# Kernel optimization log

Hardware: AMD Instinct MI355X
Metric: run time of the kernel (lower is better)

Reference implementation:

```python
import jax, jax.numpy as jnp
import numpy as np

B, C = 2048, 512          # batch, channels
CHG = 16                  # coarse grid side (16x16 -> N=256)
FHG = 16                  # fine grid side (16x16 -> F=256)
N = CHG * CHG             # coarse_span.total
F = FHG * FHG             # fine_total
K = 4                     # top4 sample mode
LOG_F = float(np.log(F))


def _ln(x, g, b, eps=1e-5):
    m = jnp.mean(x, axis=-1, keepdims=True)
    v = jnp.var(x, axis=-1, keepdims=True)
    return (x - m) * jax.lax.rsqrt(v + eps) * g + b


def _mlp3(x, w1, b1, w2, b2, w3, b3):
    # linear_stack: Linear+gelu, Linear+gelu, Linear (dropout=0 / eval)
    h = jax.nn.gelu(x @ w1 + b1)
    h = jax.nn.gelu(h @ w2 + b2)
    return h @ w3 + b3


def setup_inputs() -> dict:
    key = jax.random.key(0)
    ks = jax.random.split(key, 10)
    s = 0.02
    return {
        'x': jax.random.normal(ks[0], (B, C), jnp.float32),
        'in_g': jnp.ones((C,), jnp.float32), 'in_b': jnp.zeros((C,), jnp.float32),
        'nop_w': jax.random.normal(ks[1], (C, 1), jnp.float32) * s,
        'nop_b': jnp.zeros((1,), jnp.float32),
        'c_w1': jax.random.normal(ks[2], (C, C), jnp.float32) * s,
        'c_b1': jnp.zeros((C,), jnp.float32),
        'c_w2': jax.random.normal(ks[3], (C, C), jnp.float32) * s,
        'c_b2': jnp.zeros((C,), jnp.float32),
        'c_w3': jax.random.normal(ks[4], (C, N), jnp.float32) * s,
        'c_b3': jnp.zeros((N,), jnp.float32),
        'emb': jax.random.normal(ks[5], (N, C), jnp.float32),
        'emb_g': jnp.ones((C,), jnp.float32), 'emb_b': jnp.zeros((C,), jnp.float32),
        'f_w1': jax.random.normal(ks[6], (2 * C, C), jnp.float32) * s,
        'f_b1': jnp.zeros((C,), jnp.float32),
        'f_w2': jax.random.normal(ks[7], (C, C), jnp.float32) * s,
        'f_b2': jnp.zeros((C,), jnp.float32),
        'f_w3': jax.random.normal(ks[8], (C, F), jnp.float32) * s,
        'f_b3': jnp.zeros((F,), jnp.float32),
    }


def reference(x, in_g, in_b, nop_w, nop_b, c_w1, c_b1, c_w2, c_b2, c_w3, c_b3,
              emb, emb_g, emb_b, f_w1, f_b1, f_w2, f_b2, f_w3, f_b3):
    xn = _ln(x, in_g, in_b)                                  # (B,C)
    no_op = xn @ nop_w + nop_b                               # (B,1)
    coarse = _mlp3(xn, c_w1, c_b1, c_w2, c_b2, c_w3, c_b3)   # (B,N)
    _, idx = jax.lax.top_k(coarse, K)                        # (B,K) int32
    e = _ln(emb[idx], emb_g, emb_b)                          # (B,K,C)
    fin = jnp.concatenate([jnp.broadcast_to(xn[:, None, :], (B, K, C)), e], axis=-1)
    fine = _mlp3(fin, f_w1, f_b1, f_w2, f_b2, f_w3, f_b3)    # (B,K,F)
    # scatter value: coarse[b,i] - log F + fine + log F - lse(fine) = coarse[b,i] + log_softmax(fine)
    vals = jnp.take_along_axis(coarse, idx, axis=1)[:, :, None] + jax.nn.log_softmax(fine, axis=-1)
    dense = jnp.broadcast_to((coarse - LOG_F)[:, :, None], (B, N, F))
    dense = dense.at[jnp.arange(B)[:, None], idx].set(vals)  # top-k indices are distinct
    # view (B, ch0, ch1, fh0, fh1) -> permute (0,1,3,2,4) -> flatten
    xname = dense.reshape(B, CHG, CHG, FHG, FHG).transpose(0, 1, 3, 2, 4).reshape(B, -1)
    return jnp.concatenate([no_op, xname], axis=-1)          # (B, 1 + N*F)
```

## Files before the change

### kernel.cpp

```cpp
#include <hip/hip_runtime.h>
#include <math.h>

#define BATCH 2048
#define CH 512
#define N_COARSE 256
#define F_FINE 256
#define K_TOP 4
#define OUT_STRIDE 65537

typedef unsigned short ushort_t;
typedef __bf16 bf16x8 __attribute__((ext_vector_type(8)));
typedef float f32x4 __attribute__((ext_vector_type(4)));

__device__ __forceinline__ float gelu_tanh(float x) {
    float x3 = x * x * x;
    float t = tanhf(0.7978845608028654f * (x + 0.044715f * x3));
    return 0.5f * x * (1.0f + t);
}

__device__ __forceinline__ ushort_t f2bf(float f) {
    unsigned u = __float_as_uint(f);
    unsigned r = (u + 0x7FFF + ((u >> 16) & 1)) >> 16;
    return (ushort_t)r;
}

__global__ __launch_bounds__(256) void ln_noop_kernel(
    const float* __restrict__ x, const float* __restrict__ g, const float* __restrict__ b,
    const float* __restrict__ nop_w, const float* __restrict__ nop_b,
    float* __restrict__ xn, ushort_t* __restrict__ xn_bf, float* __restrict__ out)
{
    int row = blockIdx.x;
    int t = threadIdx.x;
    int lane = t & 63, wave = t >> 6;
    const float* xr = x + (size_t)row * CH;
    float v0 = xr[t], v1 = xr[t + 256];
    float s = v0 + v1, ss = v0 * v0 + v1 * v1;
    #pragma unroll
    for (int off = 32; off; off >>= 1) { s += __shfl_xor(s, off); ss += __shfl_xor(ss, off); }
    __shared__ float red[8];
    if (lane == 0) { red[wave] = s; red[4 + wave] = ss; }
    __syncthreads();
    s = red[0] + red[1] + red[2] + red[3];
    ss = red[4] + red[5] + red[6] + red[7];
    float mean = s * (1.0f / CH);
    float var = ss * (1.0f / CH) - mean * mean;
    float rsq = rsqrtf(var + 1e-5f);
    float xn0 = (v0 - mean) * rsq * g[t] + b[t];
    float xn1 = (v1 - mean) * rsq * g[t + 256] + b[t + 256];
    float* xnr = xn + (size_t)row * CH;
    xnr[t] = xn0; xnr[t + 256] = xn1;
    ushort_t* xbr = xn_bf + (size_t)row * CH;
    xbr[t] = f2bf(xn0); xbr[t + 256] = f2bf(xn1);
    float d = xn0 * nop_w[t] + xn1 * nop_w[t + 256];
    #pragma unroll
    for (int off = 32; off; off >>= 1) d += __shfl_xor(d, off);
    __syncthreads();
    if (lane == 0) red[wave] = d;
    __syncthreads();
    if (t == 0) out[(size_t)row * OUT_STRIDE] = red[0] + red[1] + red[2] + red[3] + nop_b[0];
}

__global__ __launch_bounds__(256) void emb_ln_kernel(
    const float* __restrict__ emb, const float* __restrict__ g, const float* __restrict__ b,
    const int* __restrict__ idx, ushort_t* __restrict__ e_bf)
{
    int blk = blockIdx.x;
    int t = threadIdx.x;
    int lane = t & 63, wave = t >> 6;
    int n = idx[blk];
    const float* er = emb + (size_t)n * CH;
    float v0 = er[t], v1 = er[t + 256];
    float s = v0 + v1, ss = v0 * v0 + v1 * v1;
    #pragma unroll
    for (int off = 32; off; off >>= 1) { s += __shfl_xor(s, off); ss += __shfl_xor(ss, off); }
    __shared__ float red[8];
    if (lane == 0) { red[wave] = s; red[4 + wave] = ss; }
    __syncthreads();
    s = red[0] + red[1] + red[2] + red[3];
    ss = red[4] + red[5] + red[6] + red[7];
    float mean = s * (1.0f / CH);
    float var = ss * (1.0f / CH) - mean * mean;
    float rsq = rsqrtf(var + 1e-5f);
    ushort_t* orow = e_bf + (size_t)blk * CH;
    orow[t] = f2bf((v0 - mean) * rsq * g[t] + b[t]);
    orow[t + 256] = f2bf((v1 - mean) * rsq * g[t + 256] + b[t + 256]);
}

__global__ __launch_bounds__(256) void convT_kernel(
    const float* __restrict__ W, ushort_t* __restrict__ Wt, int Kd, int Nd)
{
    __shared__ float s[32][33];
    int tx = threadIdx.x & 31, ty = threadIdx.x >> 5;
    int n0 = blockIdx.x * 32, k0 = blockIdx.y * 32;
    #pragma unroll
    for (int i = 0; i < 4; ++i) {
        int r = ty + i * 8;
        s[r][tx] = W[(size_t)(k0 + r) * Nd + n0 + tx];
    }
    __syncthreads();
    #pragma unroll
    for (int i = 0; i < 4; ++i) {
        int r = ty + i * 8;
        Wt[(size_t)(n0 + r) * Kd + k0 + tx] = f2bf(s[tx][r]);
    }
}

template<bool GELU>
__global__ __launch_bounds__(256) void gemm_kernel(
    const float* __restrict__ A, const float* __restrict__ W,
    const float* __restrict__ bias, float* __restrict__ Cmat, int M, int Nd, int Kd)
{
    __shared__ float As[16][68];
    __shared__ float Ws[16][68];
    int tid = threadIdx.x;
    int tx = tid & 15, ty = tid >> 4;
    int n0 = blockIdx.x * 64, m0 = blockIdx.y * 64;

    int lm = tid >> 2;
    int lk = (tid & 3) * 4;
    int wn = (tid & 15) * 4;
    int wk = tid >> 4;

    const float* Aptr = A + (size_t)(m0 + lm) * Kd + lk;
    const float* Wptr = W + (size_t)wk * Nd + n0 + wn;

    float acc[4][4] = {};

    for (int k0 = 0; k0 < Kd; k0 += 16) {
        float4 av = *(const float4*)(Aptr + k0);
        float4 wv = *(const float4*)(Wptr + (size_t)k0 * Nd);
        As[lk + 0][lm] = av.x; As[lk + 1][lm] = av.y;
        As[lk + 2][lm] = av.z; As[lk + 3][lm] = av.w;
        *(float4*)&Ws[wk][wn] = wv;
        __syncthreads();
        #pragma unroll
        for (int kk = 0; kk < 16; ++kk) {
            float4 a = *(const float4*)&As[kk][ty * 4];
            float4 w = *(const float4*)&Ws[kk][tx * 4];
            acc[0][0] += a.x * w.x; acc[0][1] += a.x * w.y; acc[0][2] += a.x * w.z; acc[0][3] += a.x * w.w;
            acc[1][0] += a.y * w.x; acc[1][1] += a.y * w.y; acc[1][2] += a.y * w.z; acc[1][3] += a.y * w.w;
            acc[2][0] += a.z * w.x; acc[2][1] += a.z * w.y; acc[2][2] += a.z * w.z; acc[2][3] += a.z * w.w;
            acc[3][0] += a.w * w.x; acc[3][1] += a.w * w.y; acc[3][2] += a.w * w.z; acc[3][3] += a.w * w.w;
        }
        __syncthreads();
    }

    #pragma unroll
    for (int i = 0; i < 4; ++i) {
        int gm = m0 + ty * 4 + i;
        int gn0 = n0 + tx * 4;
        float4 o;
        float* po = &o.x;
        #pragma unroll
        for (int j = 0; j < 4; ++j) {
            float v = acc[i][j] + bias[gn0 + j];
            if (GELU) v = gelu_tanh(v);
            po[j] = v;
        }
        *(float4*)&Cmat[(size_t)gm * Nd + gn0] = o;
    }
}

template<bool CONCAT, bool GELU, bool OUT_BF16>
__global__ __launch_bounds__(256) void mfma_gemm_kernel(
    const ushort_t* __restrict__ A1, const ushort_t* __restrict__ A2, int K1,
    const ushort_t* __restrict__ Wt, const float* __restrict__ bias,
    void* __restrict__ Cout, int M, int Nd, int Ktot)
{
    __shared__ ushort_t As[128 * 32];
    __shared__ ushort_t Bs[128 * 32];
    int t = threadIdx.x;
    int n0 = blockIdx.x * 128, m0 = blockIdx.y * 128;
    int wave = t >> 6, lane = t & 63;
    int wm = (wave & 1) * 64, wn = (wave >> 1) * 64;
    int lr = lane & 15, quad = lane >> 4;

    f32x4 acc[4][4] = {};

    for (int k0 = 0; k0 < Ktot; k0 += 32) {
        #pragma unroll
        for (int j = 0; j < 2; ++j) {
            int c = j * 256 + t;
            int r = c >> 2, q = (c & 3) * 8;
            const ushort_t* ap;
            int gr = m0 + r;
            if (CONCAT) {
                ap = (k0 < K1) ? A1 + (size_t)(gr >> 2) * K1 + k0 + q
                               : A2 + (size_t)gr * (Ktot - K1) + (k0 - K1) + q;
            } else {
                ap = A1 + (size_t)gr * Ktot + k0 + q;
            }
            *(float4*)&As[c * 8] = *(const float4*)ap;
            *(float4*)&Bs[c * 8] = *(const float4*)(Wt + (size_t)(n0 + r) * Ktot + k0 + q);
        }
        __syncthreads();
        bf16x8 af[4], bfr[4];
        #pragma unroll
        for (int i = 0; i < 4; ++i)
            af[i] = *(const bf16x8*)&As[(wm + i * 16 + lr) * 32 + quad * 8];
        #pragma unroll
        for (int j = 0; j < 4; ++j)
            bfr[j] = *(const bf16x8*)&Bs[(wn + j * 16 + lr) * 32 + quad * 8];
        #pragma unroll
        for (int i = 0; i < 4; ++i)
            #pragma unroll
            for (int j = 0; j < 4; ++j)
                acc[i][j] = __builtin_amdgcn_mfma_f32_16x16x32_bf16(af[i], bfr[j], acc[i][j], 0, 0, 0);
        __syncthreads();
    }

    #pragma unroll
    for (int j = 0; j < 4; ++j) {
        int col = n0 + wn + j * 16 + lr;
        float bv = bias[col];
        #pragma unroll
        for (int i = 0; i < 4; ++i) {
            #pragma unroll
            for (int r = 0; r < 4; ++r) {
                int row = m0 + wm + i * 16 + quad * 4 + r;
                float val = acc[i][j][r] + bv;
                if (GELU) val = gelu_tanh(val);
                if (OUT_BF16)
                    ((ushort_t*)Cout)[(size_t)row * Nd + col] = f2bf(val);
                else
                    ((float*)Cout)[(size_t)row * Nd + col] = val;
            }
        }
    }
}

__global__ __launch_bounds__(64) void topk_kernel(
    const float* __restrict__ coarse, int* __restrict__ idx, float* __restrict__ cvals)
{
    int row = blockIdx.x;
    int lane = threadIdx.x;
    const float* cr = coarse + (size_t)row * N_COARSE;
    float v[4]; int id[4];
    #pragma unroll
    for (int j = 0; j < 4; ++j) { v[j] = cr[lane + 64 * j]; id[j] = lane + 64 * j; }
    #pragma unroll
    for (int r = 0; r < K_TOP; ++r) {
        float bv = v[0]; int bi = id[0];
        #pragma unroll
        for (int j = 1; j < 4; ++j)
            if (v[j] > bv || (v[j] == bv && id[j] < bi)) { bv = v[j]; bi = id[j]; }
        #pragma unroll
        for (int off = 32; off; off >>= 1) {
            float ov = __shfl_xor(bv, off); int oi = __shfl_xor(bi, off);
            if (ov > bv || (ov == bv && oi < bi)) { bv = ov; bi = oi; }
        }
        if ((bi & 63) == lane) v[bi >> 6] = -INFINITY;
        if (lane == 0) { idx[row * K_TOP + r] = bi; cvals[row * K_TOP + r] = bv; }
    }
}

__global__ __launch_bounds__(64) void logsm_kernel(
    float* __restrict__ fine, const float* __restrict__ cvals)
{
    int row = blockIdx.x;
    int lane = threadIdx.x;
    float* fr = fine + (size_t)row * F_FINE;
    float v[4];
    #pragma unroll
    for (int j = 0; j < 4; ++j) v[j] = fr[lane + 64 * j];
    float mx = fmaxf(fmaxf(v[0], v[1]), fmaxf(v[2], v[3]));
    #pragma unroll
    for (int off = 32; off; off >>= 1) mx = fmaxf(mx, __shfl_xor(mx, off));
    float se = 0.f;
    #pragma unroll
    for (int j = 0; j < 4; ++j) se += expf(v[j] - mx);
    #pragma unroll
    for (int off = 32; off; off >>= 1) se += __shfl_xor(se, off);
    float addc = cvals[row] - mx - logf(se);
    #pragma unroll
    for (int j = 0; j < 4; ++j) fr[lane + 64 * j] = v[j] + addc;
}

__global__ __launch_bounds__(256) void scatter_kernel(
    const float* __restrict__ coarse, const float* __restrict__ fine,
    const int* __restrict__ idx, float* __restrict__ out)
{
    const float LOG_F = 5.545177444479562f;
    int b = blockIdx.y;
    int o = (blockIdx.x * 256 + threadIdx.x) * 4;
    int c0 = o >> 12, f0 = (o >> 8) & 15, c1 = (o >> 4) & 15, f1 = o & 15;
    int n = c0 * 16 + c1;
    int f = f0 * 16 + f1;
    int i0 = idx[b * 4 + 0], i1 = idx[b * 4 + 1], i2 = idx[b * 4 + 2], i3 = idx[b * 4 + 3];
    int k = -1;
    if (n == i0) k = 0; else if (n == i1) k = 1; else if (n == i2) k = 2; else if (n == i3) k = 3;
    float r0, r1, r2, r3;
    if (k >= 0) {
        const float* fr = fine + ((size_t)(b * 4 + k)) * F_FINE + f;
        r0 = fr[0]; r1 = fr[1]; r2 = fr[2]; r3 = fr[3];
    } else {
        float base = coarse[(size_t)b * N_COARSE + n] - LOG_F;
        r0 = r1 = r2 = r3 = base;
    }
    size_t ob = (size_t)b * OUT_STRIDE + 1 + o;
    out[ob + 0] = r0; out[ob + 1] = r1; out[ob + 2] = r2; out[ob + 3] = r3;
}

extern "C" void kernel_launch(void* const* d_in, const int* in_sizes, int n_in,
                              void* d_out, int out_size, void* d_ws, size_t ws_size,
                              hipStream_t stream) {
    const float* x     = (const float*)d_in[0];
    const float* in_g  = (const float*)d_in[1];
    const float* in_b  = (const float*)d_in[2];
    const float* nop_w = (const float*)d_in[3];
    const float* nop_b = (const float*)d_in[4];
    const float* c_w1  = (const float*)d_in[5];
    const float* c_b1  = (const float*)d_in[6];
    const float* c_w2  = (const float*)d_in[7];
    const float* c_b2  = (const float*)d_in[8];
    const float* c_w3  = (const float*)d_in[9];
    const float* c_b3  = (const float*)d_in[10];
    const float* emb   = (const float*)d_in[11];
    const float* emb_g = (const float*)d_in[12];
    const float* emb_b = (const float*)d_in[13];
    const float* f_w1  = (const float*)d_in[14];
    const float* f_b1  = (const float*)d_in[15];
    const float* f_w2  = (const float*)d_in[16];
    const float* f_b2  = (const float*)d_in[17];
    const float* f_w3  = (const float*)d_in[18];
    const float* f_b3  = (const float*)d_in[19];

    float* ws = (float*)d_ws;
    float* xn      = ws;
    float* h1      = xn + 1048576;
    float* h2      = h1 + 1048576;
    float* coarse  = h2 + 1048576;
    float* fine    = coarse + 524288;
    ushort_t* xn_bf  = (ushort_t*)(fine + 2097152);
    ushort_t* e_bf   = xn_bf + 1048576;
    ushort_t* fh1_bf = e_bf + 4194304;
    ushort_t* fh2_bf = fh1_bf + 4194304;
    ushort_t* wt1    = fh2_bf + 4194304;
    ushort_t* wt2    = wt1 + 524288;
    ushort_t* wt3    = wt2 + 262144;
    int*   idxb   = (int*)(wt3 + 131072);
    float* cvals  = (float*)(idxb + 8192);

    float* out = (float*)d_out;

    convT_kernel<<<dim3(16, 32), 256, 0, stream>>>(f_w1, wt1, 1024, 512);
    convT_kernel<<<dim3(16, 16), 256, 0, stream>>>(f_w2, wt2, 512, 512);
    convT_kernel<<<dim3(8, 16), 256, 0, stream>>>(f_w3, wt3, 512, 256);

    ln_noop_kernel<<<BATCH, 256, 0, stream>>>(x, in_g, in_b, nop_w, nop_b, xn, xn_bf, out);
    gemm_kernel<true><<<dim3(8, 32), 256, 0, stream>>>(xn, c_w1, c_b1, h1, 2048, 512, 512);
    gemm_kernel<true><<<dim3(8, 32), 256, 0, stream>>>(h1, c_w2, c_b2, h2, 2048, 512, 512);
    gemm_kernel<false><<<dim3(4, 32), 256, 0, stream>>>(h2, c_w3, c_b3, coarse, 2048, 256, 512);
    topk_kernel<<<BATCH, 64, 0, stream>>>(coarse, idxb, cvals);
    emb_ln_kernel<<<BATCH * K_TOP, 256, 0, stream>>>(emb, emb_g, emb_b, idxb, e_bf);
    mfma_gemm_kernel<true, true, true><<<dim3(4, 64), 256, 0, stream>>>(
        xn_bf, e_bf, 512, wt1, f_b1, fh1_bf, 8192, 512, 1024);
    mfma_gemm_kernel<false, true, true><<<dim3(4, 64), 256, 0, stream>>>(
        fh1_bf, nullptr, 0, wt2, f_b2, fh2_bf, 8192, 512, 512);
    mfma_gemm_kernel<false, false, false><<<dim3(2, 64), 256, 0, stream>>>(
        fh2_bf, nullptr, 0, wt3, f_b3, fine, 8192, 256, 512);
    logsm_kernel<<<BATCH * K_TOP, 64, 0, stream>>>(fine, cvals);
    scatter_kernel<<<dim3(64, BATCH), 256, 0, stream>>>(coarse, fine, idxb, out);
}
```

Before: 813.6 us.

## Double-buffer GEMMs, fuse topk with embedding LN, merge weight transposes

Adds register-staged double buffering to the fp32 SIMT GEMM (K tile raised to 32) and to the bf16 MFMA GEMM, so global loads for the next tile overlap compute and one barrier per step is removed. Fuses top-k selection with the embedding gather+layernorm into one kernel using vectorized loads and packed bf16 stores. Merges the three weight-transpose launches into one, gives the last fine GEMM a 64x128 tile for more blocks, and makes the output scatter use nontemporal stores. Shared memory per block roughly doubles, which may lower occupancy.

```diff
diff --git a/kernel.cpp b/kernel.cpp
--- a/kernel.cpp
+++ b/kernel.cpp
@@ -60,38 +60,18 @@
     if (t == 0) out[(size_t)row * OUT_STRIDE] = red[0] + red[1] + red[2] + red[3] + nop_b[0];
 }
 
-__global__ __launch_bounds__(256) void emb_ln_kernel(
-    const float* __restrict__ emb, const float* __restrict__ g, const float* __restrict__ b,
-    const int* __restrict__ idx, ushort_t* __restrict__ e_bf)
-{
+__global__ __launch_bounds__(256) void convT_all_kernel(
+    const float* __restrict__ w1, const float* __restrict__ w2, const float* __restrict__ w3,
+    ushort_t* __restrict__ t1, ushort_t* __restrict__ t2, ushort_t* __restrict__ t3)
+{
+    __shared__ float s[32][33];
     int blk = blockIdx.x;
-    int t = threadIdx.x;
-    int lane = t & 63, wave = t >> 6;
-    int n = idx[blk];
-    const float* er = emb + (size_t)n * CH;
-    float v0 = er[t], v1 = er[t + 256];
-    float s = v0 + v1, ss = v0 * v0 + v1 * v1;
-    #pragma unroll
-    for (int off = 32; off; off >>= 1) { s += __shfl_xor(s, off); ss += __shfl_xor(ss, off); }
-    __shared__ float red[8];
-    if (lane == 0) { red[wave] = s; red[4 + wave] = ss; }
-    __syncthreads();
-    s = red[0] + red[1] + red[2] + red[3];
-    ss = red[4] + red[5] + red[6] + red[7];
-    float mean = s * (1.0f / CH);
-    float var = ss * (1.0f / CH) - mean * mean;
-    float rsq = rsqrtf(var + 1e-5f);
-    ushort_t* orow = e_bf + (size_t)blk * CH;
-    orow[t] = f2bf((v0 - mean) * rsq * g[t] + b[t]);
-    orow[t + 256] = f2bf((v1 - mean) * rsq * g[t + 256] + b[t + 256]);
-}
-
-__global__ __launch_bounds__(256) void convT_kernel(
-    const float* __restrict__ W, ushort_t* __restrict__ Wt, int Kd, int Nd)
-{
-    __shared__ float s[32][33];
+    const float* W; ushort_t* Wt; int Kd, Nd, gx, gy;
+    if (blk < 512)      { W = w1; Wt = t1; Kd = 1024; Nd = 512; gx = blk & 15; gy = blk >> 4; }
+    else if (blk < 768) { W = w2; Wt = t2; Kd = 512;  Nd = 512; gx = (blk - 512) & 15; gy = (blk - 512) >> 4; }
+    else                { W = w3; Wt = t3; Kd = 512;  Nd = 256; gx = (blk - 768) & 7;  gy = (blk - 768) >> 3; }
     int tx = threadIdx.x & 31, ty = threadIdx.x >> 5;
-    int n0 = blockIdx.x * 32, k0 = blockIdx.y * 32;
+    int n0 = gx * 32, k0 = gy * 32;
     #pragma unroll
     for (int i = 0; i < 4; ++i) {
         int r = ty + i * 8;
@@ -108,41 +88,61 @@
 template<bool GELU>
 __global__ __launch_bounds__(256) void gemm_kernel(
     const float* __restrict__ A, const float* __restrict__ W,
-    const float* __restrict__ bias, float* __restrict__ Cmat, int M, int Nd, int Kd)
-{
-    __shared__ float As[16][68];
-    __shared__ float Ws[16][68];
-    int tid = threadIdx.x;
-    int tx = tid & 15, ty = tid >> 4;
+    const float* __restrict__ bias, float* __restrict__ Cmat, int Nd, int Kd)
+{
+    __shared__ float As[2][32][68];
+    __shared__ float Ws[2][32][68];
+    int t = threadIdx.x;
+    int tx = t & 15, ty = t >> 4;
     int n0 = blockIdx.x * 64, m0 = blockIdx.y * 64;
 
-    int lm = tid >> 2;
-    int lk = (tid & 3) * 4;
-    int wn = (tid & 15) * 4;
-    int wk = tid >> 4;
-
-    const float* Aptr = A + (size_t)(m0 + lm) * Kd + lk;
-    const float* Wptr = W + (size_t)wk * Nd + n0 + wn;
-
+    float4 aR[2], wR[2];
     float acc[4][4] = {};
 
-    for (int k0 = 0; k0 < Kd; k0 += 16) {
-        float4 av = *(const float4*)(Aptr + k0);
-        float4 wv = *(const float4*)(Wptr + (size_t)k0 * Nd);
-        As[lk + 0][lm] = av.x; As[lk + 1][lm] = av.y;
-        As[lk + 2][lm] = av.z; As[lk + 3][lm] = av.w;
-        *(float4*)&Ws[wk][wn] = wv;
+    auto loadAB = [&](int k0) {
+        #pragma unroll
+        for (int i = 0; i < 2; ++i) {
+            int c = i * 256 + t;
+            aR[i] = *(const float4*)&A[(size_t)(m0 + (c >> 3)) * Kd + k0 + (c & 7) * 4];
+        }
+        #pragma unroll
+        for (int i = 0; i < 2; ++i) {
+            int c = i * 256 + t;
+            wR[i] = *(const float4*)&W[(size_t)(k0 + (c >> 4)) * Nd + n0 + (c & 15) * 4];
+        }
+    };
+    auto storeAB = [&](int p) {
+        #pragma unroll
+        for (int i = 0; i < 2; ++i) {
+            int c = i * 256 + t, r = c >> 3, kq = (c & 7) * 4;
+            As[p][kq + 0][r] = aR[i].x; As[p][kq + 1][r] = aR[i].y;
+            As[p][kq + 2][r] = aR[i].z; As[p][kq + 3][r] = aR[i].w;
+        }
+        #pragma unroll
+        for (int i = 0; i < 2; ++i) {
+            int c = i * 256 + t;
+            *(float4*)&Ws[p][c >> 4][(c & 15) * 4] = wR[i];
+        }
+    };
+
+    loadAB(0);
+    storeAB(0);
+    int steps = Kd >> 5;
+    int p = 0;
+    for (int s = 0; s < steps; ++s) {
         __syncthreads();
-        #pragma unroll
-        for (int kk = 0; kk < 16; ++kk) {
-            float4 a = *(const float4*)&As[kk][ty * 4];
-            float4 w = *(const float4*)&Ws[kk][tx * 4];
+        if (s + 1 < steps) loadAB((s + 1) * 32);
+        #pragma unroll
+        for (int kk = 0; kk < 32; ++kk) {
+            float4 a = *(const float4*)&As[p][kk][ty * 4];
+            float4 w = *(const float4*)&Ws[p][kk][tx * 4];
             acc[0][0] += a.x * w.x; acc[0][1] += a.x * w.y; acc[0][2] += a.x * w.z; acc[0][3] += a.x * w.w;
             acc[1][0] += a.y * w.x; acc[1][1] += a.y * w.y; acc[1][2] += a.y * w.z; acc[1][3] += a.y * w.w;
             acc[2][0] += a.z * w.x; acc[2][1] += a.z * w.y; acc[2][2] += a.z * w.z; acc[2][3] += a.z * w.w;
             acc[3][0] += a.w * w.x; acc[3][1] += a.w * w.y; acc[3][2] += a.w * w.z; acc[3][3] += a.w * w.w;
         }
-        __syncthreads();
+        if (s + 1 < steps) storeAB(p ^ 1);
+        p ^= 1;
     }
 
     #pragma unroll
@@ -161,60 +161,78 @@
     }
 }
 
-template<bool CONCAT, bool GELU, bool OUT_BF16>
+template<int MT, int NT, bool CONCAT, bool GELU, bool OUT_BF16>
 __global__ __launch_bounds__(256) void mfma_gemm_kernel(
     const ushort_t* __restrict__ A1, const ushort_t* __restrict__ A2, int K1,
     const ushort_t* __restrict__ Wt, const float* __restrict__ bias,
-    void* __restrict__ Cout, int M, int Nd, int Ktot)
-{
-    __shared__ ushort_t As[128 * 32];
-    __shared__ ushort_t Bs[128 * 32];
+    void* __restrict__ Cout, int Nd, int Ktot)
+{
+    constexpr int AI = MT * 4 / 256, BI = NT * 4 / 256;
+    constexpr int FI = MT / 32, FJ = NT / 32;
+    __shared__ ushort_t As[2][MT * 32];
+    __shared__ ushort_t Bs[2][NT * 32];
     int t = threadIdx.x;
-    int n0 = blockIdx.x * 128, m0 = blockIdx.y * 128;
+    int n0 = blockIdx.x * NT, m0 = blockIdx.y * MT;
     int wave = t >> 6, lane = t & 63;
-    int wm = (wave & 1) * 64, wn = (wave >> 1) * 64;
+    int wm = (wave & 1) * (MT / 2), wn = (wave >> 1) * (NT / 2);
     int lr = lane & 15, quad = lane >> 4;
 
-    f32x4 acc[4][4] = {};
-
-    for (int k0 = 0; k0 < Ktot; k0 += 32) {
-        #pragma unroll
-        for (int j = 0; j < 2; ++j) {
-            int c = j * 256 + t;
-            int r = c >> 2, q = (c & 3) * 8;
+    f32x4 acc[FI][FJ] = {};
+    float4 aReg[AI], bReg[BI];
+
+    auto loadAB = [&](int k0) {
+        #pragma unroll
+        for (int i = 0; i < AI; ++i) {
+            int c = i * 256 + t, r = c >> 2, q = (c & 3) * 8;
+            int gr = m0 + r;
             const ushort_t* ap;
-            int gr = m0 + r;
-            if (CONCAT) {
-                ap = (k0 < K1) ? A1 + (size_t)(gr >> 2) * K1 + k0 + q
-                               : A2 + (size_t)gr * (Ktot - K1) + (k0 - K1) + q;
-            } else {
-                ap = A1 + (size_t)gr * Ktot + k0 + q;
-            }
-            *(float4*)&As[c * 8] = *(const float4*)ap;
-            *(float4*)&Bs[c * 8] = *(const float4*)(Wt + (size_t)(n0 + r) * Ktot + k0 + q);
-        }
+            if (CONCAT) ap = (k0 < K1) ? A1 + (size_t)(gr >> 2) * K1 + k0 + q
+                                       : A2 + (size_t)gr * (Ktot - K1) + (k0 - K1) + q;
+            else        ap = A1 + (size_t)gr * Ktot + k0 + q;
+            aReg[i] = *(const float4*)ap;
+        }
+        #pragma unroll
+        for (int i = 0; i < BI; ++i) {
+            int c = i * 256 + t, r = c >> 2, q = (c & 3) * 8;
+            bReg[i] = *(const float4*)(Wt + (size_t)(n0 + r) * Ktot + k0 + q);
+        }
+    };
+    auto storeAB = [&](int p) {
+        #pragma unroll
+        for (int i = 0; i < AI; ++i) { int c = i * 256 + t; *(float4*)&As[p][c * 8] = aReg[i]; }
+        #pragma unroll
+        for (int i = 0; i < BI; ++i) { int c = i * 256 + t; *(float4*)&Bs[p][c * 8] = bReg[i]; }
+    };
+
+    loadAB(0);
+    storeAB(0);
+    int steps = Ktot >> 5;
+    int p = 0;
+    for (int s = 0; s < steps; ++s) {
         __syncthreads();
-        bf16x8 af[4], bfr[4];
-        #pragma unroll
-        for (int i = 0; i < 4; ++i)
-            af[i] = *(const bf16x8*)&As[(wm + i * 16 + lr) * 32 + quad * 8];
-        #pragma unroll
-        for (int j = 0; j < 4; ++j)
-            bfr[j] = *(const bf16x8*)&Bs[(wn + j * 16 + lr) * 32 + quad * 8];
-        #pragma unroll
-        for (int i = 0; i < 4; ++i)
+        if (s + 1 < steps) loadAB((s + 1) * 32);
+        bf16x8 af[FI], bfr[FJ];
+        #pragma unroll
+        for (int i = 0; i < FI; ++i)
+            af[i] = *(const bf16x8*)&As[p][(wm + i * 16 + lr) * 32 + quad * 8];
+        #pragma unroll
+        for (int j = 0; j < FJ; ++j)
+            bfr[j] = *(const bf16x8*)&Bs[p][(wn + j * 16 + lr) * 32 + quad * 8];
+        #pragma unroll
+        for (int i = 0; i < FI; ++i)
             #pragma unroll
-            for (int j = 0; j < 4; ++j)
+            for (int j = 0; j < FJ; ++j)
                 acc[i][j] = __builtin_amdgcn_mfma_f32_16x16x32_bf16(af[i], bfr[j], acc[i][j], 0, 0, 0);
-        __syncthreads();
-    }
-
-    #pragma unroll
-    for (int j = 0; j < 4; ++j) {
+        if (s + 1 < steps) storeAB(p ^ 1);
+        p ^= 1;
+    }
+
+    #pragma unroll
+    for (int j = 0; j < FJ; ++j) {
         int col = n0 + wn + j * 16 + lr;
         float bv = bias[col];
         #pragma unroll
-        for (int i = 0; i < 4; ++i) {
+        for (int i = 0; i < FI; ++i) {
             #pragma unroll
             for (int r = 0; r < 4; ++r) {
                 int row = m0 + wm + i * 16 + quad * 4 + r;
@@ -229,29 +247,66 @@
     }
 }
 
-__global__ __launch_bounds__(64) void topk_kernel(
-    const float* __restrict__ coarse, int* __restrict__ idx, float* __restrict__ cvals)
-{
-    int row = blockIdx.x;
-    int lane = threadIdx.x;
-    const float* cr = coarse + (size_t)row * N_COARSE;
-    float v[4]; int id[4];
-    #pragma unroll
-    for (int j = 0; j < 4; ++j) { v[j] = cr[lane + 64 * j]; id[j] = lane + 64 * j; }
-    #pragma unroll
-    for (int r = 0; r < K_TOP; ++r) {
-        float bv = v[0]; int bi = id[0];
-        #pragma unroll
-        for (int j = 1; j < 4; ++j)
-            if (v[j] > bv || (v[j] == bv && id[j] < bi)) { bv = v[j]; bi = id[j]; }
-        #pragma unroll
-        for (int off = 32; off; off >>= 1) {
-            float ov = __shfl_xor(bv, off); int oi = __shfl_xor(bi, off);
-            if (ov > bv || (ov == bv && oi < bi)) { bv = ov; bi = oi; }
-        }
-        if ((bi & 63) == lane) v[bi >> 6] = -INFINITY;
-        if (lane == 0) { idx[row * K_TOP + r] = bi; cvals[row * K_TOP + r] = bv; }
-    }
+__global__ __launch_bounds__(256) void topk_embln_kernel(
+    const float* __restrict__ coarse, const float* __restrict__ emb,
+    const float* __restrict__ g, const float* __restrict__ b,
+    int* __restrict__ idx, float* __restrict__ cvals, ushort_t* __restrict__ e_bf)
+{
+    int brow = blockIdx.x;
+    int t = threadIdx.x;
+    int wave = t >> 6, lane = t & 63;
+    __shared__ int sidx[4];
+
+    if (wave == 0) {
+        const float* cr = coarse + (size_t)brow * N_COARSE;
+        float v[4]; int id[4];
+        #pragma unroll
+        for (int j = 0; j < 4; ++j) { v[j] = cr[lane + 64 * j]; id[j] = lane + 64 * j; }
+        #pragma unroll
+        for (int r = 0; r < K_TOP; ++r) {
+            float bv = v[0]; int bi = id[0];
+            #pragma unroll
+            for (int j = 1; j < 4; ++j)
+                if (v[j] > bv || (v[j] == bv && id[j] < bi)) { bv = v[j]; bi = id[j]; }
+            #pragma unroll
+            for (int off = 32; off; off >>= 1) {
+                float ov = __shfl_xor(bv, off); int oi = __shfl_xor(bi, off);
+                if (ov > bv || (ov == bv && oi < bi)) { bv = ov; bi = oi; }
+            }
+            if ((bi & 63) == lane) v[bi >> 6] = -INFINITY;
+            if (lane == 0) {
+                sidx[r] = bi;
+                idx[brow * K_TOP + r] = bi;
+                cvals[brow * K_TOP + r] = bv;
+            }
+        }
+    }
+    __syncthreads();
+
+    int n = sidx[wave];
+    const float* er = emb + (size_t)n * CH + lane * 8;
+    float4 u0 = *(const float4*)er;
+    float4 u1 = *(const float4*)(er + 4);
+    float s  = u0.x + u0.y + u0.z + u0.w + u1.x + u1.y + u1.z + u1.w;
+    float ss = u0.x * u0.x + u0.y * u0.y + u0.z * u0.z + u0.w * u0.w
+             + u1.x * u1.x + u1.y * u1.y + u1.z * u1.z + u1.w * u1.w;
+    #pragma unroll
+    for (int off = 32; off; off >>= 1) { s += __shfl_xor(s, off); ss += __shfl_xor(ss, off); }
+    float mean = s * (1.0f / CH);
+    float var = ss * (1.0f / CH) - mean * mean;
+    float rsq = rsqrtf(var + 1e-5f);
+    float4 g0 = *(const float4*)(g + lane * 8), g1 = *(const float4*)(g + lane * 8 + 4);
+    float4 b0 = *(const float4*)(b + lane * 8), b1 = *(const float4*)(b + lane * 8 + 4);
+    uint4 pk;
+    pk.x = (unsigned)f2bf((u0.x - mean) * rsq * g0.x + b0.x) |
+           ((unsigned)f2bf((u0.y - mean) * rsq * g0.y + b0.y) << 16);
+    pk.y = (unsigned)f2bf((u0.z - mean) * rsq * g0.z + b0.z) |
+           ((unsigned)f2bf((u0.w - mean) * rsq * g0.w + b0.w) << 16);
+    pk.z = (unsigned)f2bf((u1.x - mean) * rsq * g1.x + b1.x) |
+           ((unsigned)f2bf((u1.y - mean) * rsq * g1.y + b1.y) << 16);
+    pk.w = (unsigned)f2bf((u1.z - mean) * rsq * g1.z + b1.z) |
+           ((unsigned)f2bf((u1.w - mean) * rsq * g1.w + b1.w) << 16);
+    *(uint4*)(e_bf + (size_t)(brow * K_TOP + wave) * CH + lane * 8) = pk;
 }
 
 __global__ __launch_bounds__(64) void logsm_kernel(
@@ -298,7 +353,10 @@
         r0 = r1 = r2 = r3 = base;
     }
     size_t ob = (size_t)b * OUT_STRIDE + 1 + o;
-    out[ob + 0] = r0; out[ob + 1] = r1; out[ob + 2] = r2; out[ob + 3] = r3;
+    __builtin_nontemporal_store(r0, &out[ob + 0]);
+    __builtin_nontemporal_store(r1, &out[ob + 1]);
+    __builtin_nontemporal_store(r2, &out[ob + 2]);
+    __builtin_nontemporal_store(r3, &out[ob + 3]);
 }
 
 extern "C" void kernel_launch(void* const* d_in, const int* in_sizes, int n_in,
@@ -343,22 +401,18 @@
 
     float* out = (float*)d_out;
 
-    convT_kernel<<<dim3(16, 32), 256, 0, stream>>>(f_w1, wt1, 1024, 512);
-    convT_kernel<<<dim3(16, 16), 256, 0, stream>>>(f_w2, wt2, 512, 512);
-    convT_kernel<<<dim3(8, 16), 256, 0, stream>>>(f_w3, wt3, 512, 256);
-
+    convT_all_kernel<<<896, 256, 0, stream>>>(f_w1, f_w2, f_w3, wt1, wt2, wt3);
     ln_noop_kernel<<<BATCH, 256, 0, stream>>>(x, in_g, in_b, nop_w, nop_b, xn, xn_bf, out);
-    gemm_kernel<true><<<dim3(8, 32), 256, 0, stream>>>(xn, c_w1, c_b1, h1, 2048, 512, 512);
-    gemm_kernel<true><<<dim3(8, 32), 256, 0, stream>>>(h1, c_w2, c_b2, h2, 2048, 512, 512);
-    gemm_kernel<false><<<dim3(4, 32), 256, 0, stream>>>(h2, c_w3, c_b3, coarse, 2048, 256, 512);
-    topk_kernel<<<BATCH, 64, 0, stream>>>(coarse, idxb, cvals);
-    emb_ln_kernel<<<BATCH * K_TOP, 256, 0, stream>>>(emb, emb_g, emb_b, idxb, e_bf);
-    mfma_gemm_kernel<true, true, true><<<dim3(4, 64), 256, 0, stream>>>(
-        xn_bf, e_bf, 512, wt1, f_b1, fh1_bf, 8192, 512, 1024);
-    mfma_gemm_kernel<false, true, true><<<dim3(4, 64), 256, 0, stream>>>(
-        fh1_bf, nullptr, 0, wt2, f_b2, fh2_bf, 8192, 512, 512);
-    mfma_gemm_kernel<false, false, false><<<dim3(2, 64), 256, 0, stream>>>(
-        fh2_bf, nullptr, 0, wt3, f_b3, fine, 8192, 256, 512);
+    gemm_kernel<true><<<dim3(8, 32), 256, 0, stream>>>(xn, c_w1, c_b1, h1, 512, 512);
+    gemm_kernel<true><<<dim3(8, 32), 256, 0, stream>>>(h1, c_w2, c_b2, h2, 512, 512);
+    gemm_kernel<false><<<dim3(4, 32), 256, 0, stream>>>(h2, c_w3, c_b3, coarse, 256, 512);
+    topk_embln_kernel<<<BATCH, 256, 0, stream>>>(coarse, emb, emb_g, emb_b, idxb, cvals, e_bf);
+    mfma_gemm_kernel<128, 128, true, true, true><<<dim3(4, 64), 256, 0, stream>>>(
+        xn_bf, e_bf, 512, wt1, f_b1, fh1_bf, 512, 1024);
+    mfma_gemm_kernel<128, 128, false, true, true><<<dim3(4, 64), 256, 0, stream>>>(
+        fh1_bf, nullptr, 0, wt2, f_b2, fh2_bf, 512, 512);
+    mfma_gemm_kernel<64, 128, false, false, false><<<dim3(2, 128), 256, 0, stream>>>(
+        fh2_bf, nullptr, 0, wt3, f_b3, fine, 256, 512);
     logsm_kernel<<<BATCH * K_TOP, 64, 0, stream>>>(fine, cvals);
     scatter_kernel<<<dim3(64, BATCH), 256, 0, stream>>>(coarse, fine, idxb, out);
 }
```

New measurement: 800.4 us. No clear change (-1.6%).
